# Kernel tuning notes

Hardware: AMD Instinct MI355X
Metric: run time of the kernel (lower is better)

The kernel has to match this reference:

```python
import jax, jax.numpy as jnp
import numpy as np

WS = 7       # window_size
SHIFT = 3    # shift_size
NH = 4       # num_heads


def _layernorm(x, g, b, eps=1e-5):
    m = jnp.mean(x, axis=-1, keepdims=True)
    v = jnp.mean((x - m) ** 2, axis=-1, keepdims=True)
    return (x - m) * jax.lax.rsqrt(v + eps) * g + b


def _mha(x, wq, bq, wk, bk, wv, bv, wo, bo):
    # x: [n, s, c]; weights stored as [in, out]
    n, s, c = x.shape
    dk = c // NH
    q = (x @ wq + bq).reshape(n, s, NH, dk).transpose(0, 2, 1, 3)
    k = (x @ wk + bk).reshape(n, s, NH, dk).transpose(0, 2, 1, 3)
    v = (x @ wv + bv).reshape(n, s, NH, dk).transpose(0, 2, 1, 3)
    scores = jnp.einsum('nhqd,nhkd->nhqk', q, k) / jnp.sqrt(jnp.float32(dk))
    attn = jax.nn.softmax(scores, axis=-1)  # dropout is identity in eval
    out = jnp.einsum('nhqk,nhkd->nhqd', attn, v)
    out = out.transpose(0, 2, 1, 3).reshape(n, s, c)
    return out @ wo + bo


def _window_partition(x):
    B, H, W, C = x.shape
    x = x.reshape(B, H // WS, WS, W // WS, WS, C)
    x = x.transpose(0, 1, 3, 2, 4, 5)
    return x.reshape(-1, WS * WS, C)


def _window_reverse(wins, H, W):
    C = wins.shape[-1]
    B = wins.shape[0] // ((H // WS) * (W // WS))
    x = wins.reshape(B, H // WS, W // WS, WS, WS, C)
    x = x.transpose(0, 1, 3, 2, 4, 5)
    return x.reshape(B, H, W, C)


def setup_inputs() -> dict:
    key = jax.random.key(0)
    ks = jax.random.split(key, 16)
    C = 128
    def w(k, shape):
        return jax.random.normal(k, shape, dtype=jnp.float32) * 0.02
    return {
        'x':  jax.random.normal(ks[0], (4, 56, 56, C), dtype=jnp.float32),
        'wq': w(ks[1], (C, C)), 'bq': jnp.zeros((C,), jnp.float32),
        'wk': w(ks[2], (C, C)), 'bk': jnp.zeros((C,), jnp.float32),
        'wv': w(ks[3], (C, C)), 'bv': jnp.zeros((C,), jnp.float32),
        'wo': w(ks[4], (C, C)), 'bo': jnp.zeros((C,), jnp.float32),
        'w1': w(ks[5], (C, 4 * C)), 'b1': jnp.zeros((4 * C,), jnp.float32),
        'w2': w(ks[6], (4 * C, C)), 'b2': jnp.zeros((C,), jnp.float32),
        'g1': jnp.ones((C,), jnp.float32), 'be1': jnp.zeros((C,), jnp.float32),
        'g2': jnp.ones((C,), jnp.float32), 'be2': jnp.zeros((C,), jnp.float32),
    }


def reference(x, wq, bq, wk, bk, wv, bv, wo, bo, w1, b1, w2, b2, g1, be1, g2, be2):
    B, H, W, C = x.shape
    # cyclic shift
    xs = jnp.roll(x, shift=(-SHIFT, -SHIFT), axis=(1, 2)) if SHIFT > 0 else x
    # windowed attention (note: original code replaces x, no residual here)
    wins = _window_partition(xs)                         # [B*nW, 49, C]
    attn_wins = _mha(wins, wq, bq, wk, bk, wv, bv, wo, bo)
    xs = _window_reverse(attn_wins, H, W)
    x = jnp.roll(xs, shift=(SHIFT, SHIFT), axis=(1, 2)) if SHIFT > 0 else xs
    # global attention residual branch (flatten H*W tokens)
    xf = x.reshape(B, H * W, C)
    xf = xf + _mha(_layernorm(xf, g1, be1), wq, bq, wk, bk, wv, bv, wo, bo)
    # MLP residual branch
    h = jax.nn.gelu(_layernorm(xf, g2, be2) @ w1 + b1, approximate=False)
    xf = xf + (h @ w2 + b2)
    return xf.reshape(B, H, W, C)
```

## Files before the change

### kernel.cpp

```cpp
#include <hip/hip_runtime.h>
#include <hip/hip_bf16.h>
#include <math.h>

#define NH 4
#define DK 32
#define CC 128
#define HW 56
#define SHIFT 3
#define NTOK 12544
#define S_GLB 3136
#define VTW_STRIDE 12608
#define SCALE_L2E 0.25503488f

typedef unsigned short u16;
typedef short bf16x8 __attribute__((ext_vector_type(8)));
typedef unsigned short u16x8 __attribute__((ext_vector_type(8)));
typedef float f32x4 __attribute__((ext_vector_type(4)));

static __device__ __forceinline__ u16 f2bf(float f) {
  unsigned int b = __builtin_bit_cast(unsigned int, f);
  return (u16)((b + 0x7FFFu + ((b >> 16) & 1u)) >> 16);
}
static __device__ __forceinline__ unsigned pk2bf(float a, float b) {
  unsigned r;
  asm("v_cvt_pk_bf16_f32 %0, %1, %2" : "=v"(r) : "v"(a), "v"(b));
  return r;
}
static __device__ __forceinline__ float fexp2(float x) {
  float r;
  asm("v_exp_f32 %0, %1" : "=v"(r) : "v"(x));
  return r;
}
static __device__ __forceinline__ void gload16(const void* g, void* l) {
  __builtin_amdgcn_global_load_lds(
      (const __attribute__((address_space(1))) unsigned int*)g,
      (__attribute__((address_space(3))) unsigned int*)l, 16, 0, 0);
}

__global__ __launch_bounds__(256) void prep_k(
    const float* __restrict__ w1, const float* __restrict__ w2,
    const float* __restrict__ wq, const float* __restrict__ wk,
    const float* __restrict__ wv, const float* __restrict__ wo,
    const float* __restrict__ x,
    u16* __restrict__ w1t, u16* __restrict__ w2t,
    u16* __restrict__ wqkvt, u16* __restrict__ wot, u16* __restrict__ xg) {
  if (blockIdx.x < 768) {
    const int idx = blockIdx.x * 256 + threadIdx.x;
    if (idx < 65536) {
      const int c = idx >> 7, r = idx & 127;
      w1t[idx] = f2bf(w1[r * 512 + c]);
    } else if (idx < 131072) {
      const int o = idx - 65536;
      const int c = o / 512, r = o - c * 512;
      w2t[o] = f2bf(w2[r * 128 + c]);
    } else {
      const int o = idx - 131072;
      const int which = o >> 14, oo = o & 16383;
      const int c = oo >> 7, r = oo & 127;
      const float* src = (which == 0) ? wq : (which == 1) ? wk : (which == 2) ? wv : wo;
      u16* dst = (which < 3) ? (wqkvt + which * 16384) : wot;
      dst[oo] = f2bf(src[r * 128 + c]);
    }
  } else {
    const int bid = blockIdx.x - 768;
    const int t = bid * 2 + (threadIdx.x >> 7);
    const int c = threadIdx.x & 127;
    const int win = t / 49, tok = t % 49;
    const int b = win >> 6, wrem = win & 63;
    const int wi = wrem >> 3, wj = wrem & 7;
    const int i = tok / 7, j = tok % 7;
    int hh = wi * 7 + i + SHIFT; if (hh >= HW) hh -= HW;
    int ww = wj * 7 + j + SHIFT; if (ww >= HW) ww -= HW;
    xg[(size_t)t * CC + c] = f2bf(x[((size_t)(b * HW + hh) * HW + ww) * CC + c]);
  }
}

template <int PATH>
__global__ __launch_bounds__(256) void qkv_gemm_k(
    const u16* __restrict__ xin, const u16* __restrict__ wqkvt,
    const float* __restrict__ bq, const float* __restrict__ bk,
    const float* __restrict__ bv,
    u16* __restrict__ qo, u16* __restrict__ ko, u16* __restrict__ vto) {
  __shared__ __align__(16) u16 xs[64][136];
  __shared__ __align__(16) u16 wt[64][136];
  const int tid = threadIdx.x;
  const int w = tid >> 6, lane = tid & 63;
  const int lo = lane & 15, hi = lane >> 4, hi4 = hi * 4;
  const int m0 = blockIdx.x * 64;
  const int widx = blockIdx.y >> 1;
  const int n0 = (blockIdx.y & 1) * 64;
  {
    const int r = tid >> 2, sg = tid & 3;
    const u16* sx = &xin[(size_t)(m0 + r) * CC + sg * 32];
    const u16* sw = &wqkvt[(size_t)widx * CC * CC + (size_t)(n0 + r) * CC + sg * 32];
#pragma unroll
    for (int j = 0; j < 4; ++j) {
      *reinterpret_cast<u16x8*>(&xs[r][sg * 32 + j * 8]) = *reinterpret_cast<const u16x8*>(&sx[j * 8]);
      *reinterpret_cast<u16x8*>(&wt[r][sg * 32 + j * 8]) = *reinterpret_cast<const u16x8*>(&sw[j * 8]);
    }
  }
  __syncthreads();
  if (widx < 2) {
    const float* bias = (widx == 0) ? bq : bk;
    u16* outp = (widx == 0) ? qo : ko;
    const float oscale = (widx == 0) ? SCALE_L2E : 1.0f;
    f32x4 acc[4];
#pragma unroll
    for (int st = 0; st < 4; ++st) {
      const float b_ = bias[n0 + st * 16 + lo];
      acc[st] = (f32x4){b_, b_, b_, b_};
    }
#pragma unroll
    for (int kk = 0; kk < 4; ++kk) {
      const bf16x8 af = *reinterpret_cast<const bf16x8*>(&xs[w * 16 + lo][kk * 32 + 8 * hi]);
#pragma unroll
      for (int st = 0; st < 4; ++st) {
        const bf16x8 bfr = *reinterpret_cast<const bf16x8*>(&wt[st * 16 + lo][kk * 32 + 8 * hi]);
        acc[st] = __builtin_amdgcn_mfma_f32_16x16x32_bf16(af, bfr, acc[st], 0, 0, 0);
      }
    }
#pragma unroll
    for (int r = 0; r < 4; ++r) {
      const int mm = m0 + w * 16 + hi4 + r;
      size_t rowbase, hstride;
      if (PATH == 0) {
        const int win = mm / 49, tok = mm - win * 49;
        rowbase = ((size_t)(win * 4) * 49 + tok) * DK;
        hstride = (size_t)49 * DK;
      } else {
        const int b = mm / S_GLB, s = mm - b * S_GLB;
        rowbase = ((size_t)(b * 4) * S_GLB + s) * DK;
        hstride = (size_t)S_GLB * DK;
      }
#pragma unroll
      for (int st = 0; st < 4; ++st) {
        const int c = n0 + st * 16 + lo, h = c >> 5, d = c & 31;
        outp[rowbase + (size_t)h * hstride + d] = f2bf(acc[st][r] * oscale);
      }
    }
  } else {
    f32x4 bias4;
#pragma unroll
    for (int r = 0; r < 4; ++r) bias4[r] = bv[n0 + w * 16 + hi4 + r];
    f32x4 acc[4];
#pragma unroll
    for (int st = 0; st < 4; ++st) acc[st] = bias4;
#pragma unroll
    for (int kk = 0; kk < 4; ++kk) {
      const bf16x8 af = *reinterpret_cast<const bf16x8*>(&wt[w * 16 + lo][kk * 32 + 8 * hi]);
#pragma unroll
      for (int st = 0; st < 4; ++st) {
        const bf16x8 bfr = *reinterpret_cast<const bf16x8*>(&xs[st * 16 + lo][kk * 32 + 8 * hi]);
        acc[st] = __builtin_amdgcn_mfma_f32_16x16x32_bf16(af, bfr, acc[st], 0, 0, 0);
      }
    }
#pragma unroll
    for (int st = 0; st < 4; ++st) {
      const int mm = m0 + st * 16 + lo;
#pragma unroll
      for (int r = 0; r < 4; ++r) {
        const int c = n0 + w * 16 + hi4 + r;
        if (PATH == 0) {
          vto[(size_t)c * VTW_STRIDE + mm] = f2bf(acc[st][r]);
        } else {
          const int b = mm / S_GLB, s = mm - b * S_GLB;
          vto[((size_t)b * CC + c) * S_GLB + s] = f2bf(acc[st][r]);
        }
      }
    }
  }
}

__global__ __launch_bounds__(256) void win_attn_k(
    const u16* __restrict__ qw, const u16* __restrict__ kw,
    const u16* __restrict__ vtw, u16* __restrict__ aow) {
  __shared__ __align__(16) u16 psh[4][16][72];
  const int tid = threadIdx.x;
  const int wvi = tid >> 6, lane = tid & 63;
  const int lo = lane & 15, hi = lane >> 4, hi4 = hi * 4;
  const int wh = blockIdx.x * 4 + wvi;
  const int win = wh >> 2, hd = wh & 3;
  const f32x4 zero4 = {0.f, 0.f, 0.f, 0.f};
  bf16x8 ones;
#pragma unroll
  for (int j = 0; j < 8; ++j) ones[j] = (short)0x3F80;

  bf16x8 kf[4], vf[2][2];
#pragma unroll
  for (int st = 0; st < 4; ++st)
    kf[st] = *reinterpret_cast<const bf16x8*>(&kw[((size_t)wh * 49 + st * 16 + lo) * DK + 8 * hi]);
#pragma unroll
  for (int dst = 0; dst < 2; ++dst)
#pragma unroll
    for (int kch = 0; kch < 2; ++kch)
      vf[dst][kch] = *reinterpret_cast<const bf16x8*>(
          &vtw[(size_t)(hd * DK + dst * 16 + lo) * VTW_STRIDE + win * 49 + kch * 32 + 8 * hi]);

#pragma unroll
  for (int g = 0; g < 4; ++g) {
    const bf16x8 qf = *reinterpret_cast<const bf16x8*>(
        &qw[((size_t)wh * 49 + g * 16 + lo) * DK + 8 * hi]);
    f32x4 s4[4];
#pragma unroll
    for (int st = 0; st < 4; ++st) {
      s4[st] = __builtin_amdgcn_mfma_f32_16x16x32_bf16(kf[st], qf, zero4, 0, 0, 0);
#pragma unroll
      for (int r = 0; r < 4; ++r)
        if (st * 16 + hi4 + r >= 49) s4[st][r] = -1e30f;
    }
#pragma unroll
    for (int st = 0; st < 4; ++st) {
      uint2 pk;
      pk.x = pk2bf(fexp2(s4[st][0]), fexp2(s4[st][1]));
      pk.y = pk2bf(fexp2(s4[st][2]), fexp2(s4[st][3]));
      *reinterpret_cast<uint2*>(&psh[wvi][lo][st * 16 + hi4]) = pk;
    }
    asm volatile("" ::: "memory");
    f32x4 acc0 = zero4, acc1 = zero4, lacc = zero4;
#pragma unroll
    for (int kch = 0; kch < 2; ++kch) {
      const bf16x8 pa = *reinterpret_cast<const bf16x8*>(&psh[wvi][lo][kch * 32 + 8 * hi]);
      acc0 = __builtin_amdgcn_mfma_f32_16x16x32_bf16(pa, vf[0][kch], acc0, 0, 0, 0);
      acc1 = __builtin_amdgcn_mfma_f32_16x16x32_bf16(pa, vf[1][kch], acc1, 0, 0, 0);
      lacc = __builtin_amdgcn_mfma_f32_16x16x32_bf16(pa, ones, lacc, 0, 0, 0);
    }
#pragma unroll
    for (int r = 0; r < 4; ++r) {
      const int qrow = g * 16 + hi4 + r;
      if (qrow < 49) {
        const float rl = 1.0f / lacc[r];
        const size_t tw = (size_t)win * 49 + qrow;
        aow[tw * CC + hd * DK + lo] = f2bf(acc0[r] * rl);
        aow[tw * CC + hd * DK + 16 + lo] = f2bf(acc1[r] * rl);
      }
    }
  }
}

__global__ __launch_bounds__(256) void glb_attn_k(
    const u16* __restrict__ qg, const u16* __restrict__ kg,
    const u16* __restrict__ vtg, float* __restrict__ po, float* __restrict__ pl) {
  __shared__ __align__(16) u16 ksh[2][64][32];
  __shared__ __align__(16) u16 vtsh[2][32][64];
  __shared__ __align__(16) u16 psh[4][16][64];
  const int tid = threadIdx.x;
  const int w = tid >> 6, lane = tid & 63;
  const int lo = lane & 15, hi = lane >> 4, hi4 = hi * 4;
  const int wg = blockIdx.x;
  const int sid = (wg & 7) * 196 + (wg >> 3);
  const int sp = sid / 784;
  const int rem = sid - sp * 784;
  const int bh = rem / 49;
  const int q0 = (rem - bh * 49) * 64;
  const int kt_beg = sp * 25;
  const int kt_end = sp ? 49 : 25;
  const f32x4 zero4 = {0.f, 0.f, 0.f, 0.f};
  bf16x8 ones;
#pragma unroll
  for (int j = 0; j < 8; ++j) ones[j] = (short)0x3F80;

  const bf16x8 qfrag = *reinterpret_cast<const bf16x8*>(
      &qg[((size_t)bh * S_GLB + q0 + w * 16 + lo) * DK + 8 * hi]);
  const u16* kg0 = kg + (size_t)bh * S_GLB * DK;
  const u16* vg0 = vtg + (size_t)bh * DK * S_GLB;

  const u16* ksrc = kg0 + (size_t)(w * 16 + (lane >> 2)) * DK + (lane & 3) * 8;
  const u16* vsrc = vg0 + (size_t)(w * 8 + (lane >> 3)) * S_GLB + ((lane & 7) ^ (lane >> 3)) * 8;
  u16* kdst0 = &ksh[0][w * 16][0]; u16* kdst1 = &ksh[1][w * 16][0];
  u16* vdst0 = &vtsh[0][w * 8][0]; u16* vdst1 = &vtsh[1][w * 8][0];

  f32x4 oacc0 = zero4, oacc1 = zero4, lacc = zero4;

  gload16(ksrc + (size_t)kt_beg * 64 * DK, kdst0);
  gload16(vsrc + (size_t)kt_beg * 64, vdst0);
  __syncthreads();

  char* const pbase = (char*)&psh[w][lo][0];
  char* const vbase0 = (char*)&vtsh[0][0][0];
  const unsigned swz = (unsigned)(lo & 7) << 4;

  for (int kt = kt_beg; kt < kt_end; ++kt) {
    const int cur = (kt - kt_beg) & 1;
    if (kt + 1 < kt_end) {
      gload16(ksrc + (size_t)(kt + 1) * 64 * DK, cur ? kdst0 : kdst1);
      gload16(vsrc + (size_t)(kt + 1) * 64, cur ? vdst0 : vdst1);
    }
    f32x4 s4[4];
    __builtin_amdgcn_s_setprio(1);
#pragma unroll
    for (int st = 0; st < 4; ++st) {
      const bf16x8 kfrag = *reinterpret_cast<const bf16x8*>(&ksh[cur][st * 16 + lo][8 * hi]);
      s4[st] = __builtin_amdgcn_mfma_f32_16x16x32_bf16(kfrag, qfrag, zero4, 0, 0, 0);
    }
    __builtin_amdgcn_s_setprio(0);
#pragma unroll
    for (int st = 0; st < 4; ++st) {
      uint2 pk;
      pk.x = pk2bf(fexp2(s4[st][0]), fexp2(s4[st][1]));
      pk.y = pk2bf(fexp2(s4[st][2]), fexp2(s4[st][3]));
      *reinterpret_cast<uint2*>(pbase + (((unsigned)(st * 32 + hi * 8)) ^ swz)) = pk;
    }
    asm volatile("" ::: "memory");
    char* const vrow0 = vbase0 + (size_t)cur * (32 * 64 * 2) + lo * 128;
    __builtin_amdgcn_s_setprio(1);
#pragma unroll
    for (int kch = 0; kch < 2; ++kch) {
      const unsigned off = ((unsigned)(kch * 64 + hi * 16)) ^ swz;
      const bf16x8 pa = *reinterpret_cast<const bf16x8*>(pbase + off);
      const bf16x8 v0 = *reinterpret_cast<const bf16x8*>(vrow0 + off);
      const bf16x8 v1 = *reinterpret_cast<const bf16x8*>(vrow0 + 16 * 128 + off);
      oacc0 = __builtin_amdgcn_mfma_f32_16x16x32_bf16(pa, v0, oacc0, 0, 0, 0);
      oacc1 = __builtin_amdgcn_mfma_f32_16x16x32_bf16(pa, v1, oacc1, 0, 0, 0);
      lacc = __builtin_amdgcn_mfma_f32_16x16x32_bf16(pa, ones, lacc, 0, 0, 0);
    }
    __builtin_amdgcn_s_setprio(0);
    __syncthreads();
  }

  const int b = bh >> 2, hd = bh & 3;
  float* pob = po + (size_t)sp * NTOK * CC;
#pragma unroll
  for (int r = 0; r < 4; ++r) {
    const size_t t = (size_t)b * S_GLB + q0 + w * 16 + hi4 + r;
    pob[t * CC + hd * DK + lo] = oacc0[r];
    pob[t * CC + hd * DK + 16 + lo] = oacc1[r];
    if (lo == 0)
      pl[((size_t)sp * 16 + bh) * S_GLB + q0 + w * 16 + hi4 + r] = lacc[r];
  }
}

template <int MODE>
__global__ __launch_bounds__(256) void proj_ln_k(
    const u16* __restrict__ ain, const float* __restrict__ po,
    const float* __restrict__ pl, const u16* __restrict__ wot,
    const float* __restrict__ bo, const float* __restrict__ resid,
    const float* __restrict__ lng, const float* __restrict__ lnb,
    float* __restrict__ xfo, u16* __restrict__ ybf) {
  __shared__ __align__(16) u16 xs[64][136];
  __shared__ __align__(16) u16 wt[128][136];
  const int tid = threadIdx.x;
  const int w = tid >> 6, lane = tid & 63;
  const int lo = lane & 15, hi = lane >> 4, hi4 = hi * 4;
  const int m0 = blockIdx.x * 64;
  {
    const int r = tid >> 2, sg = tid & 3;
    if (MODE == 0) {
      const u16* sx = &ain[(size_t)(m0 + r) * CC + sg * 32];
#pragma unroll
      for (int j = 0; j < 4; ++j)
        *reinterpret_cast<u16x8*>(&xs[r][sg * 32 + j * 8]) = *reinterpret_cast<const u16x8*>(&sx[j * 8]);
    } else {
      const int mm = m0 + r;
      const int b = mm / S_GLB, s_ = mm - b * S_GLB;
      const float l0 = pl[((size_t)(b * 4 + sg)) * S_GLB + s_];
      const float l1 = pl[((size_t)(16 + b * 4 + sg)) * S_GLB + s_];
      const float rl = 1.0f / (l0 + l1);
      const float* pa = &po[(size_t)mm * CC + sg * 32];
      const float* pb = pa + (size_t)NTOK * CC;
#pragma unroll
      for (int j = 0; j < 32; j += 4) {
        const float4 a4 = *reinterpret_cast<const float4*>(&pa[j]);
        const float4 b4 = *reinterpret_cast<const float4*>(&pb[j]);
        uint2 pk;
        pk.x = pk2bf((a4.x + b4.x) * rl, (a4.y + b4.y) * rl);
        pk.y = pk2bf((a4.z + b4.z) * rl, (a4.w + b4.w) * rl);
        *reinterpret_cast<uint2*>(&xs[r][sg * 32 + j]) = pk;
      }
    }
    const int r2 = tid >> 1, sg2 = tid & 1;
    const u16* sw = &wot[(size_t)r2 * CC + sg2 * 64];
#pragma unroll
    for (int j = 0; j < 8; ++j)
      *reinterpret_cast<u16x8*>(&wt[r2][sg2 * 64 + j * 8]) = *reinterpret_cast<const u16x8*>(&sw[j * 8]);
  }
  __syncthreads();
  f32x4 acc[8];
#pragma unroll
  for (int st = 0; st < 8; ++st) {
    const float b_ = bo[st * 16 + lo];
    acc[st] = (f32x4){b_, b_, b_, b_};
  }
#pragma unroll
  for (int kk = 0; kk < 4; ++kk) {
    const bf16x8 af = *reinterpret_cast<const bf16x8*>(&xs[w * 16 + lo][kk * 32 + 8 * hi]);
#pragma unroll
    for (int st = 0; st < 8; ++st) {
      const bf16x8 bfr = *reinterpret_cast<const bf16x8*>(&wt[st * 16 + lo][kk * 32 + 8 * hi]);
      acc[st] = __builtin_amdgcn_mfma_f32_16x16x32_bf16(af, bfr, acc[st], 0, 0, 0);
    }
  }
  float gv[8], bv2[8];
#pragma unroll
  for (int st = 0; st < 8; ++st) { gv[st] = lng[st * 16 + lo]; bv2[st] = lnb[st * 16 + lo]; }
#pragma unroll
  for (int r = 0; r < 4; ++r) {
    const int mm = m0 + w * 16 + hi4 + r;
    size_t trow;
    if (MODE == 0) {
      const int win = mm / 49, tok = mm - win * 49;
      const int b = win >> 6, wi = (win >> 3) & 7, wj = win & 7;
      const int ii = tok / 7, jj = tok - ii * 7;
      int hr = wi * 7 + ii + SHIFT; if (hr >= HW) hr -= HW;
      int wr = wj * 7 + jj + SHIFT; if (wr >= HW) wr -= HW;
      trow = (size_t)b * S_GLB + hr * HW + wr;
    } else {
      trow = (size_t)mm;
    }
    float v[8];
    float s = 0.f, sq = 0.f;
#pragma unroll
    for (int st = 0; st < 8; ++st) {
      float t_ = acc[st][r];
      if (MODE == 1) t_ += resid[trow * CC + st * 16 + lo];
      v[st] = t_;
      s += t_;
      sq += t_ * t_;
    }
    s += __shfl_xor(s, 1); s += __shfl_xor(s, 2); s += __shfl_xor(s, 4); s += __shfl_xor(s, 8);
    sq += __shfl_xor(sq, 1); sq += __shfl_xor(sq, 2); sq += __shfl_xor(sq, 4); sq += __shfl_xor(sq, 8);
    const float mu = s * 0.0078125f;
    const float rsig = rsqrtf(sq * 0.0078125f - mu * mu + 1e-5f);
#pragma unroll
    for (int st = 0; st < 8; ++st) {
      const size_t idx = trow * CC + st * 16 + lo;
      xfo[idx] = v[st];
      ybf[idx] = f2bf((v[st] - mu) * rsig * gv[st] + bv2[st]);
    }
  }
}

__global__ __launch_bounds__(256) void gemm1_k(
    const u16* __restrict__ ybf, const u16* __restrict__ w1t,
    const float* __restrict__ b1, u16* __restrict__ hb) {
  __shared__ __align__(16) u16 xs[64][136];
  __shared__ __align__(16) u16 wt[64][136];
  const int tid = threadIdx.x;
  const int w = tid >> 6, lane = tid & 63;
  const int lo = lane & 15, hi = lane >> 4;
  const int m0 = blockIdx.x * 64, n0 = blockIdx.y * 64;
  {
    const int r = tid >> 2, sg = tid & 3;
    const u16* src_x = &ybf[(size_t)(m0 + r) * CC + sg * 32];
    const u16* src_w = &w1t[(size_t)(n0 + r) * CC + sg * 32];
#pragma unroll
    for (int j = 0; j < 4; ++j) {
      *reinterpret_cast<u16x8*>(&xs[r][sg * 32 + j * 8]) = *reinterpret_cast<const u16x8*>(&src_x[j * 8]);
      *reinterpret_cast<u16x8*>(&wt[r][sg * 32 + j * 8]) = *reinterpret_cast<const u16x8*>(&src_w[j * 8]);
    }
  }
  __syncthreads();
  f32x4 acc[4];
#pragma unroll
  for (int st = 0; st < 4; ++st) {
    const float bv = b1[n0 + st * 16 + lo];
    acc[st] = (f32x4){bv, bv, bv, bv};
  }
#pragma unroll
  for (int kk = 0; kk < 4; ++kk) {
    const bf16x8 af = *reinterpret_cast<const bf16x8*>(&xs[w * 16 + lo][kk * 32 + 8 * hi]);
#pragma unroll
    for (int st = 0; st < 4; ++st) {
      const bf16x8 bfr = *reinterpret_cast<const bf16x8*>(&wt[st * 16 + lo][kk * 32 + 8 * hi]);
      acc[st] = __builtin_amdgcn_mfma_f32_16x16x32_bf16(af, bfr, acc[st], 0, 0, 0);
    }
  }
#pragma unroll
  for (int st = 0; st < 4; ++st) {
#pragma unroll
    for (int r = 0; r < 4; ++r) {
      const float val = acc[st][r];
      const float gel = 0.5f * val * (1.0f + erff(val * 0.70710678118f));
      hb[(size_t)(m0 + w * 16 + (hi << 2) + r) * 512 + n0 + st * 16 + lo] = f2bf(gel);
    }
  }
}

__global__ __launch_bounds__(256) void gemm2_k(
    const u16* __restrict__ hb, const u16* __restrict__ w2t,
    const float* __restrict__ b2, const float* __restrict__ xf,
    float* __restrict__ out) {
  __shared__ __align__(16) u16 xs[64][136];
  __shared__ __align__(16) u16 wt[64][136];
  const int tid = threadIdx.x;
  const int w = tid >> 6, lane = tid & 63;
  const int lo = lane & 15, hi = lane >> 4;
  const int m0 = blockIdx.x * 64, n0 = blockIdx.y * 64;
  f32x4 acc[4];
#pragma unroll
  for (int st = 0; st < 4; ++st) {
    const float bv = b2[n0 + st * 16 + lo];
    acc[st] = (f32x4){bv, bv, bv, bv};
  }
  for (int kc = 0; kc < 4; ++kc) {
    if (kc) __syncthreads();
    {
      const int r = tid >> 2, sg = tid & 3;
      const u16* src_x = &hb[(size_t)(m0 + r) * 512 + kc * 128 + sg * 32];
      const u16* src_w = &w2t[(size_t)(n0 + r) * 512 + kc * 128 + sg * 32];
#pragma unroll
      for (int j = 0; j < 4; ++j) {
        *reinterpret_cast<u16x8*>(&xs[r][sg * 32 + j * 8]) = *reinterpret_cast<const u16x8*>(&src_x[j * 8]);
        *reinterpret_cast<u16x8*>(&wt[r][sg * 32 + j * 8]) = *reinterpret_cast<const u16x8*>(&src_w[j * 8]);
      }
    }
    __syncthreads();
#pragma unroll
    for (int kk = 0; kk < 4; ++kk) {
      const bf16x8 af = *reinterpret_cast<const bf16x8*>(&xs[w * 16 + lo][kk * 32 + 8 * hi]);
#pragma unroll
      for (int st = 0; st < 4; ++st) {
        const bf16x8 bfr = *reinterpret_cast<const bf16x8*>(&wt[st * 16 + lo][kk * 32 + 8 * hi]);
        acc[st] = __builtin_amdgcn_mfma_f32_16x16x32_bf16(af, bfr, acc[st], 0, 0, 0);
      }
    }
  }
#pragma unroll
  for (int st = 0; st < 4; ++st) {
#pragma unroll
    for (int r = 0; r < 4; ++r) {
      const size_t idx = (size_t)(m0 + w * 16 + (hi << 2) + r) * CC + n0 + st * 16 + lo;
      out[idx] = xf[idx] + acc[st][r];
    }
  }
}

extern "C" void kernel_launch(void* const* d_in, const int* in_sizes, int n_in,
                              void* d_out, int out_size, void* d_ws, size_t ws_size,
                              hipStream_t stream) {
  (void)in_sizes; (void)n_in; (void)out_size; (void)ws_size;
  const float* x   = (const float*)d_in[0];
  const float* wq  = (const float*)d_in[1];
  const float* bq  = (const float*)d_in[2];
  const float* wk  = (const float*)d_in[3];
  const float* bk  = (const float*)d_in[4];
  const float* wv  = (const float*)d_in[5];
  const float* bv  = (const float*)d_in[6];
  const float* wo  = (const float*)d_in[7];
  const float* bo  = (const float*)d_in[8];
  const float* w1  = (const float*)d_in[9];
  const float* b1  = (const float*)d_in[10];
  const float* w2  = (const float*)d_in[11];
  const float* b2  = (const float*)d_in[12];
  const float* g1  = (const float*)d_in[13];
  const float* be1 = (const float*)d_in[14];
  const float* g2  = (const float*)d_in[15];
  const float* be2 = (const float*)d_in[16];
  float* out = (float*)d_out;

  char* p = (char*)d_ws;
  auto alloc = [&](size_t bytes) { char* r = p; p += (bytes + 255) & ~(size_t)255; return r; };
  float* xf  = (float*)alloc((size_t)NTOK * CC * 4);
  u16* xg    = (u16*)alloc((size_t)NTOK * CC * 2);
  u16* qw    = (u16*)alloc((size_t)NTOK * CC * 2 + 4096);
  u16* kw    = (u16*)alloc((size_t)NTOK * CC * 2 + 4096);
  u16* vtw   = (u16*)alloc((size_t)CC * VTW_STRIDE * 2);
  u16* aow   = (u16*)alloc((size_t)NTOK * CC * 2);
  u16* hb    = (u16*)alloc((size_t)NTOK * 512 * 2);
  float* po  = (float*)alloc((size_t)2 * NTOK * CC * 4);
  float* pl  = (float*)alloc((size_t)2 * 16 * S_GLB * 4);
  u16* wqkvt = (u16*)alloc(3 * 16384 * 2);
  u16* wot   = (u16*)alloc(16384 * 2);
  u16* w1t   = (u16*)alloc(65536 * 2);
  u16* w2t   = (u16*)alloc(65536 * 2);

  prep_k<<<768 + NTOK / 2, 256, 0, stream>>>(
      w1, w2, wq, wk, wv, wo, x, w1t, w2t, wqkvt, wot, xg);
  qkv_gemm_k<0><<<dim3(NTOK / 64, 6), 256, 0, stream>>>(xg, wqkvt, bq, bk, bv, qw, kw, vtw);
  win_attn_k<<<256, 256, 0, stream>>>(qw, kw, vtw, aow);
  proj_ln_k<0><<<NTOK / 64, 256, 0, stream>>>(
      aow, nullptr, nullptr, wot, bo, nullptr, g1, be1, xf, xg);
  qkv_gemm_k<1><<<dim3(NTOK / 64, 6), 256, 0, stream>>>(xg, wqkvt, bq, bk, bv, qw, kw, vtw);
  glb_attn_k<<<1568, 256, 0, stream>>>(qw, kw, vtw, po, pl);
  proj_ln_k<1><<<NTOK / 64, 256, 0, stream>>>(
      nullptr, po, pl, wot, bo, xf, g2, be2, xf, xg);
  gemm1_k<<<dim3(NTOK / 64, 8), 256, 0, stream>>>(xg, w1t, b1, hb);
  gemm2_k<<<dim3(NTOK / 64, 2), 256, 0, stream>>>(hb, w2t, b2, xf, out);
}
```

Baseline: 114.5 us.

## Retile QKV, window-attention and projection kernels; drop setprio in global attention

The QKV GEMM now computes all 128 output columns per block, halving the grid in y. This removes duplicate loads of the X tile but doubles per-wave accumulators. Window attention switches from one wave per window-head with a 4-step loop to one block per window-head, with each wave handling one 16-row query group. That quadruples the grid, and each wave redundantly loads the same K and V fragments. proj_ln is moved to 32-row tiles with 128 threads for more blocks, and the s_setprio hints in the global attention loop are removed.

```diff
diff --git a/kernel.cpp b/kernel.cpp
--- a/kernel.cpp
+++ b/kernel.cpp
@@ -82,39 +82,40 @@
     const float* __restrict__ bv,
     u16* __restrict__ qo, u16* __restrict__ ko, u16* __restrict__ vto) {
   __shared__ __align__(16) u16 xs[64][136];
-  __shared__ __align__(16) u16 wt[64][136];
+  __shared__ __align__(16) u16 wt[128][136];
   const int tid = threadIdx.x;
   const int w = tid >> 6, lane = tid & 63;
   const int lo = lane & 15, hi = lane >> 4, hi4 = hi * 4;
   const int m0 = blockIdx.x * 64;
-  const int widx = blockIdx.y >> 1;
-  const int n0 = (blockIdx.y & 1) * 64;
+  const int widx = blockIdx.y;
   {
     const int r = tid >> 2, sg = tid & 3;
     const u16* sx = &xin[(size_t)(m0 + r) * CC + sg * 32];
-    const u16* sw = &wqkvt[(size_t)widx * CC * CC + (size_t)(n0 + r) * CC + sg * 32];
-#pragma unroll
-    for (int j = 0; j < 4; ++j) {
+#pragma unroll
+    for (int j = 0; j < 4; ++j)
       *reinterpret_cast<u16x8*>(&xs[r][sg * 32 + j * 8]) = *reinterpret_cast<const u16x8*>(&sx[j * 8]);
-      *reinterpret_cast<u16x8*>(&wt[r][sg * 32 + j * 8]) = *reinterpret_cast<const u16x8*>(&sw[j * 8]);
-    }
+    const int r2 = tid >> 1, sg2 = tid & 1;
+    const u16* sw = &wqkvt[(size_t)widx * CC * CC + (size_t)r2 * CC + sg2 * 64];
+#pragma unroll
+    for (int j = 0; j < 8; ++j)
+      *reinterpret_cast<u16x8*>(&wt[r2][sg2 * 64 + j * 8]) = *reinterpret_cast<const u16x8*>(&sw[j * 8]);
   }
   __syncthreads();
   if (widx < 2) {
     const float* bias = (widx == 0) ? bq : bk;
     u16* outp = (widx == 0) ? qo : ko;
     const float oscale = (widx == 0) ? SCALE_L2E : 1.0f;
-    f32x4 acc[4];
-#pragma unroll
-    for (int st = 0; st < 4; ++st) {
-      const float b_ = bias[n0 + st * 16 + lo];
+    f32x4 acc[8];
+#pragma unroll
+    for (int st = 0; st < 8; ++st) {
+      const float b_ = bias[st * 16 + lo];
       acc[st] = (f32x4){b_, b_, b_, b_};
     }
 #pragma unroll
     for (int kk = 0; kk < 4; ++kk) {
       const bf16x8 af = *reinterpret_cast<const bf16x8*>(&xs[w * 16 + lo][kk * 32 + 8 * hi]);
 #pragma unroll
-      for (int st = 0; st < 4; ++st) {
+      for (int st = 0; st < 8; ++st) {
         const bf16x8 bfr = *reinterpret_cast<const bf16x8*>(&wt[st * 16 + lo][kk * 32 + 8 * hi]);
         acc[st] = __builtin_amdgcn_mfma_f32_16x16x32_bf16(af, bfr, acc[st], 0, 0, 0);
       }
@@ -133,38 +134,46 @@
         hstride = (size_t)S_GLB * DK;
       }
 #pragma unroll
-      for (int st = 0; st < 4; ++st) {
-        const int c = n0 + st * 16 + lo, h = c >> 5, d = c & 31;
+      for (int st = 0; st < 8; ++st) {
+        const int c = st * 16 + lo, h = c >> 5, d = c & 31;
         outp[rowbase + (size_t)h * hstride + d] = f2bf(acc[st][r] * oscale);
       }
     }
   } else {
-    f32x4 bias4;
-#pragma unroll
-    for (int r = 0; r < 4; ++r) bias4[r] = bv[n0 + w * 16 + hi4 + r];
-    f32x4 acc[4];
-#pragma unroll
-    for (int st = 0; st < 4; ++st) acc[st] = bias4;
+    f32x4 acc[2][4];
+#pragma unroll
+    for (int cg = 0; cg < 2; ++cg) {
+      f32x4 bias4;
+#pragma unroll
+      for (int r = 0; r < 4; ++r) bias4[r] = bv[cg * 64 + w * 16 + hi4 + r];
+#pragma unroll
+      for (int st = 0; st < 4; ++st) acc[cg][st] = bias4;
+    }
 #pragma unroll
     for (int kk = 0; kk < 4; ++kk) {
-      const bf16x8 af = *reinterpret_cast<const bf16x8*>(&wt[w * 16 + lo][kk * 32 + 8 * hi]);
+      const bf16x8 af0 = *reinterpret_cast<const bf16x8*>(&wt[w * 16 + lo][kk * 32 + 8 * hi]);
+      const bf16x8 af1 = *reinterpret_cast<const bf16x8*>(&wt[64 + w * 16 + lo][kk * 32 + 8 * hi]);
 #pragma unroll
       for (int st = 0; st < 4; ++st) {
         const bf16x8 bfr = *reinterpret_cast<const bf16x8*>(&xs[st * 16 + lo][kk * 32 + 8 * hi]);
-        acc[st] = __builtin_amdgcn_mfma_f32_16x16x32_bf16(af, bfr, acc[st], 0, 0, 0);
-      }
-    }
-#pragma unroll
-    for (int st = 0; st < 4; ++st) {
-      const int mm = m0 + st * 16 + lo;
-#pragma unroll
-      for (int r = 0; r < 4; ++r) {
-        const int c = n0 + w * 16 + hi4 + r;
-        if (PATH == 0) {
-          vto[(size_t)c * VTW_STRIDE + mm] = f2bf(acc[st][r]);
-        } else {
-          const int b = mm / S_GLB, s = mm - b * S_GLB;
-          vto[((size_t)b * CC + c) * S_GLB + s] = f2bf(acc[st][r]);
+        acc[0][st] = __builtin_amdgcn_mfma_f32_16x16x32_bf16(af0, bfr, acc[0][st], 0, 0, 0);
+        acc[1][st] = __builtin_amdgcn_mfma_f32_16x16x32_bf16(af1, bfr, acc[1][st], 0, 0, 0);
+      }
+    }
+#pragma unroll
+    for (int cg = 0; cg < 2; ++cg) {
+#pragma unroll
+      for (int st = 0; st < 4; ++st) {
+        const int mm = m0 + st * 16 + lo;
+#pragma unroll
+        for (int r = 0; r < 4; ++r) {
+          const int c = cg * 64 + w * 16 + hi4 + r;
+          if (PATH == 0) {
+            vto[(size_t)c * VTW_STRIDE + mm] = f2bf(acc[cg][st][r]);
+          } else {
+            const int b = mm / S_GLB, s = mm - b * S_GLB;
+            vto[((size_t)b * CC + c) * S_GLB + s] = f2bf(acc[cg][st][r]);
+          }
         }
       }
     }
@@ -176,9 +185,9 @@
     const u16* __restrict__ vtw, u16* __restrict__ aow) {
   __shared__ __align__(16) u16 psh[4][16][72];
   const int tid = threadIdx.x;
-  const int wvi = tid >> 6, lane = tid & 63;
+  const int g = tid >> 6, lane = tid & 63;
   const int lo = lane & 15, hi = lane >> 4, hi4 = hi * 4;
-  const int wh = blockIdx.x * 4 + wvi;
+  const int wh = blockIdx.x;
   const int win = wh >> 2, hd = wh & 3;
   const f32x4 zero4 = {0.f, 0.f, 0.f, 0.f};
   bf16x8 ones;
@@ -196,43 +205,40 @@
       vf[dst][kch] = *reinterpret_cast<const bf16x8*>(
           &vtw[(size_t)(hd * DK + dst * 16 + lo) * VTW_STRIDE + win * 49 + kch * 32 + 8 * hi]);
 
-#pragma unroll
-  for (int g = 0; g < 4; ++g) {
-    const bf16x8 qf = *reinterpret_cast<const bf16x8*>(
-        &qw[((size_t)wh * 49 + g * 16 + lo) * DK + 8 * hi]);
-    f32x4 s4[4];
-#pragma unroll
-    for (int st = 0; st < 4; ++st) {
-      s4[st] = __builtin_amdgcn_mfma_f32_16x16x32_bf16(kf[st], qf, zero4, 0, 0, 0);
-#pragma unroll
-      for (int r = 0; r < 4; ++r)
-        if (st * 16 + hi4 + r >= 49) s4[st][r] = -1e30f;
-    }
-#pragma unroll
-    for (int st = 0; st < 4; ++st) {
-      uint2 pk;
-      pk.x = pk2bf(fexp2(s4[st][0]), fexp2(s4[st][1]));
-      pk.y = pk2bf(fexp2(s4[st][2]), fexp2(s4[st][3]));
-      *reinterpret_cast<uint2*>(&psh[wvi][lo][st * 16 + hi4]) = pk;
-    }
-    asm volatile("" ::: "memory");
-    f32x4 acc0 = zero4, acc1 = zero4, lacc = zero4;
-#pragma unroll
-    for (int kch = 0; kch < 2; ++kch) {
-      const bf16x8 pa = *reinterpret_cast<const bf16x8*>(&psh[wvi][lo][kch * 32 + 8 * hi]);
-      acc0 = __builtin_amdgcn_mfma_f32_16x16x32_bf16(pa, vf[0][kch], acc0, 0, 0, 0);
-      acc1 = __builtin_amdgcn_mfma_f32_16x16x32_bf16(pa, vf[1][kch], acc1, 0, 0, 0);
-      lacc = __builtin_amdgcn_mfma_f32_16x16x32_bf16(pa, ones, lacc, 0, 0, 0);
-    }
-#pragma unroll
-    for (int r = 0; r < 4; ++r) {
-      const int qrow = g * 16 + hi4 + r;
-      if (qrow < 49) {
-        const float rl = 1.0f / lacc[r];
-        const size_t tw = (size_t)win * 49 + qrow;
-        aow[tw * CC + hd * DK + lo] = f2bf(acc0[r] * rl);
-        aow[tw * CC + hd * DK + 16 + lo] = f2bf(acc1[r] * rl);
-      }
+  const bf16x8 qf = *reinterpret_cast<const bf16x8*>(
+      &qw[((size_t)wh * 49 + g * 16 + lo) * DK + 8 * hi]);
+  f32x4 s4[4];
+#pragma unroll
+  for (int st = 0; st < 4; ++st) {
+    s4[st] = __builtin_amdgcn_mfma_f32_16x16x32_bf16(kf[st], qf, zero4, 0, 0, 0);
+#pragma unroll
+    for (int r = 0; r < 4; ++r)
+      if (st * 16 + hi4 + r >= 49) s4[st][r] = -1e30f;
+  }
+#pragma unroll
+  for (int st = 0; st < 4; ++st) {
+    uint2 pk;
+    pk.x = pk2bf(fexp2(s4[st][0]), fexp2(s4[st][1]));
+    pk.y = pk2bf(fexp2(s4[st][2]), fexp2(s4[st][3]));
+    *reinterpret_cast<uint2*>(&psh[g][lo][st * 16 + hi4]) = pk;
+  }
+  asm volatile("" ::: "memory");
+  f32x4 acc0 = zero4, acc1 = zero4, lacc = zero4;
+#pragma unroll
+  for (int kch = 0; kch < 2; ++kch) {
+    const bf16x8 pa = *reinterpret_cast<const bf16x8*>(&psh[g][lo][kch * 32 + 8 * hi]);
+    acc0 = __builtin_amdgcn_mfma_f32_16x16x32_bf16(pa, vf[0][kch], acc0, 0, 0, 0);
+    acc1 = __builtin_amdgcn_mfma_f32_16x16x32_bf16(pa, vf[1][kch], acc1, 0, 0, 0);
+    lacc = __builtin_amdgcn_mfma_f32_16x16x32_bf16(pa, ones, lacc, 0, 0, 0);
+  }
+#pragma unroll
+  for (int r = 0; r < 4; ++r) {
+    const int qrow = g * 16 + hi4 + r;
+    if (qrow < 49) {
+      const float rl = 1.0f / lacc[r];
+      const size_t tw = (size_t)win * 49 + qrow;
+      aow[tw * CC + hd * DK + lo] = f2bf(acc0[r] * rl);
+      aow[tw * CC + hd * DK + 16 + lo] = f2bf(acc1[r] * rl);
     }
   }
 }
@@ -286,13 +292,11 @@
       gload16(vsrc + (size_t)(kt + 1) * 64, cur ? vdst0 : vdst1);
     }
     f32x4 s4[4];
-    __builtin_amdgcn_s_setprio(1);
 #pragma unroll
     for (int st = 0; st < 4; ++st) {
       const bf16x8 kfrag = *reinterpret_cast<const bf16x8*>(&ksh[cur][st * 16 + lo][8 * hi]);
       s4[st] = __builtin_amdgcn_mfma_f32_16x16x32_bf16(kfrag, qfrag, zero4, 0, 0, 0);
     }
-    __builtin_amdgcn_s_setprio(0);
 #pragma unroll
     for (int st = 0; st < 4; ++st) {
       uint2 pk;
@@ -302,7 +306,6 @@
     }
     asm volatile("" ::: "memory");
     char* const vrow0 = vbase0 + (size_t)cur * (32 * 64 * 2) + lo * 128;
-    __builtin_amdgcn_s_setprio(1);
 #pragma unroll
     for (int kch = 0; kch < 2; ++kch) {
       const unsigned off = ((unsigned)(kch * 64 + hi * 16)) ^ swz;
@@ -313,7 +316,6 @@
       oacc1 = __builtin_amdgcn_mfma_f32_16x16x32_bf16(pa, v1, oacc1, 0, 0, 0);
       lacc = __builtin_amdgcn_mfma_f32_16x16x32_bf16(pa, ones, lacc, 0, 0, 0);
     }
-    __builtin_amdgcn_s_setprio(0);
     __syncthreads();
   }
 
@@ -330,18 +332,18 @@
 }
 
 template <int MODE>
-__global__ __launch_bounds__(256) void proj_ln_k(
+__global__ __launch_bounds__(128) void proj_ln_k(
     const u16* __restrict__ ain, const float* __restrict__ po,
     const float* __restrict__ pl, const u16* __restrict__ wot,
     const float* __restrict__ bo, const float* __restrict__ resid,
     const float* __restrict__ lng, const float* __restrict__ lnb,
     float* __restrict__ xfo, u16* __restrict__ ybf) {
-  __shared__ __align__(16) u16 xs[64][136];
+  __shared__ __align__(16) u16 xs[32][136];
   __shared__ __align__(16) u16 wt[128][136];
   const int tid = threadIdx.x;
   const int w = tid >> 6, lane = tid & 63;
   const int lo = lane & 15, hi = lane >> 4, hi4 = hi * 4;
-  const int m0 = blockIdx.x * 64;
+  const int m0 = blockIdx.x * 32;
   {
     const int r = tid >> 2, sg = tid & 3;
     if (MODE == 0) {
@@ -368,10 +370,14 @@
       }
     }
     const int r2 = tid >> 1, sg2 = tid & 1;
-    const u16* sw = &wot[(size_t)r2 * CC + sg2 * 64];
-#pragma unroll
-    for (int j = 0; j < 8; ++j)
-      *reinterpret_cast<u16x8*>(&wt[r2][sg2 * 64 + j * 8]) = *reinterpret_cast<const u16x8*>(&sw[j * 8]);
+#pragma unroll
+    for (int rr = 0; rr < 2; ++rr) {
+      const u16* sw = &wot[(size_t)(r2 + rr * 64) * CC + sg2 * 64];
+#pragma unroll
+      for (int j = 0; j < 8; ++j)
+        *reinterpret_cast<u16x8*>(&wt[r2 + rr * 64][sg2 * 64 + j * 8]) =
+            *reinterpret_cast<const u16x8*>(&sw[j * 8]);
+    }
   }
   __syncthreads();
   f32x4 acc[8];
@@ -565,13 +571,13 @@
 
   prep_k<<<768 + NTOK / 2, 256, 0, stream>>>(
       w1, w2, wq, wk, wv, wo, x, w1t, w2t, wqkvt, wot, xg);
-  qkv_gemm_k<0><<<dim3(NTOK / 64, 6), 256, 0, stream>>>(xg, wqkvt, bq, bk, bv, qw, kw, vtw);
-  win_attn_k<<<256, 256, 0, stream>>>(qw, kw, vtw, aow);
-  proj_ln_k<0><<<NTOK / 64, 256, 0, stream>>>(
+  qkv_gemm_k<0><<<dim3(NTOK / 64, 3), 256, 0, stream>>>(xg, wqkvt, bq, bk, bv, qw, kw, vtw);
+  win_attn_k<<<1024, 256, 0, stream>>>(qw, kw, vtw, aow);
+  proj_ln_k<0><<<NTOK / 32, 128, 0, stream>>>(
       aow, nullptr, nullptr, wot, bo, nullptr, g1, be1, xf, xg);
-  qkv_gemm_k<1><<<dim3(NTOK / 64, 6), 256, 0, stream>>>(xg, wqkvt, bq, bk, bv, qw, kw, vtw);
+  qkv_gemm_k<1><<<dim3(NTOK / 64, 3), 256, 0, stream>>>(xg, wqkvt, bq, bk, bv, qw, kw, vtw);
   glb_attn_k<<<1568, 256, 0, stream>>>(qw, kw, vtw, po, pl);
-  proj_ln_k<1><<<NTOK / 64, 256, 0, stream>>>(
+  proj_ln_k<1><<<NTOK / 32, 128, 0, stream>>>(
       nullptr, po, pl, wot, bo, xf, g2, be2, xf, xg);
   gemm1_k<<<dim3(NTOK / 64, 8), 256, 0, stream>>>(xg, w1t, b1, hb);
   gemm2_k<<<dim3(NTOK / 64, 2), 256, 0, stream>>>(hb, w2t, b2, xf, out);
```

After: 123.4 us. 1.08x slower.
